# Performance work log

Hardware: AMD Instinct MI355X
Metric: run time of the kernel (lower is better)

## Reference

```python
import jax, jax.numpy as jnp
import numpy as np

N_NODES = 100000
IN_DIM = 128
HID = 128
N_EDGES = 1600000
N_PAIRS = 500000


def setup_inputs() -> dict:
    key = jax.random.key(0)
    ks = jax.random.split(key, 16)

    def lin(k, fan_out, fan_in):
        s = 1.0 / np.sqrt(fan_in)
        kw, kb = jax.random.split(k)
        W = jax.random.uniform(kw, (fan_out, fan_in), jnp.float32, -s, s)
        b = jax.random.uniform(kb, (fan_out,), jnp.float32, -s, s)
        return W, b

    x = jax.random.normal(ks[0], (N_NODES, IN_DIM), jnp.float32)
    edge_index = jax.random.randint(ks[1], (2, N_EDGES), 0, N_NODES, jnp.int64)
    edge_pairs = jax.random.randint(ks[2], (N_PAIRS, 2), 0, N_NODES, jnp.int64)

    # SAGEConv 1: lin_l (neighbor aggr, with bias), lin_r (root, no bias)
    W1l, b1l = lin(ks[3], HID, IN_DIM)
    W1r, _ = lin(ks[4], HID, IN_DIM)
    # SAGEConv 2
    W2l, b2l = lin(ks[5], HID, HID)
    W2r, _ = lin(ks[6], HID, HID)
    # MLP decoder
    Wm1, bm1 = lin(ks[7], HID, HID)
    Wm2, bm2 = lin(ks[8], HID // 2, HID)
    Wm3, bm3 = lin(ks[9], 1, HID // 2)

    return dict(x=x, edge_index=edge_index, edge_pairs=edge_pairs,
                W1l=W1l, b1l=b1l, W1r=W1r,
                W2l=W2l, b2l=b2l, W2r=W2r,
                Wm1=Wm1, bm1=bm1, Wm2=Wm2, bm2=bm2, Wm3=Wm3, bm3=bm3)


def _sage_conv(x, src, dst, Wl, bl, Wr):
    # mean aggregation of source-node features into destination nodes
    msg_sum = jax.ops.segment_sum(x[src], dst, num_segments=N_NODES)  # [N, D]
    cnt = jax.ops.segment_sum(jnp.ones((src.shape[0],), x.dtype), dst,
                              num_segments=N_NODES)
    aggr = msg_sum / jnp.maximum(cnt, 1.0)[:, None]
    return aggr @ Wl.T + bl + x @ Wr.T


def reference(x, edge_index, edge_pairs,
              W1l, b1l, W1r, W2l, b2l, W2r,
              Wm1, bm1, Wm2, bm2, Wm3, bm3):
    src, dst = edge_index[0], edge_index[1]
    # encode (eval mode: dropout = identity)
    h = jax.nn.relu(_sage_conv(x, src, dst, W1l, b1l, W1r))
    z = _sage_conv(h, src, dst, W2l, b2l, W2r)  # [N, HID]
    # decode
    hp = z[edge_pairs[:, 0]] * z[edge_pairs[:, 1]]  # [P, HID]
    hp = jax.nn.relu(hp @ Wm1.T + bm1)
    hp = jax.nn.relu(hp @ Wm2.T + bm2)
    return (hp @ Wm3.T + bm3).squeeze(-1)  # [P]
```

## Files before the change

### kernel.cpp

```cpp
#include <hip/hip_runtime.h>
#include <stdint.h>

typedef _Float16 half8 __attribute__((ext_vector_type(8)));
typedef float float4v __attribute__((ext_vector_type(4)));

constexpr int kN = 100000;
constexpr int kE = 1600000;
constexpr int kP = 500000;
constexpr int NBS = (kN + 255) / 256;
constexpr int CT3 = kN / 16;
constexpr int DT2 = kP / 32;

__global__ void prep_kernel(
    const int* __restrict__ dst, int* __restrict__ deg, int* __restrict__ slot,
    const float* __restrict__ x, _Float16* __restrict__ xh,
    const float* __restrict__ W1l, const float* __restrict__ W1r,
    const float* __restrict__ W2l, const float* __restrict__ W2r,
    const float* __restrict__ Wm1, const float* __restrict__ Wm2,
    _Float16* __restrict__ CW1h, _Float16* __restrict__ CW1e,
    _Float16* __restrict__ CW2h, _Float16* __restrict__ CW2e,
    _Float16* __restrict__ M1h,  _Float16* __restrict__ M2h)
{
    const int b = blockIdx.x;
    if (b < 6250) {
        const int e = b * 256 + threadIdx.x;
        if (e < kE) slot[e] = atomicAdd(&deg[dst[e]], 1);
    } else if (b < 12500) {
        const int i = ((b - 6250) * 256 + threadIdx.x) * 8;
        if (i >= kN * 128) return;
        const float4 a = *(const float4*)&x[i];
        const float4 bb = *(const float4*)&x[i + 4];
        half8 v;
        v[0] = (_Float16)a.x;  v[1] = (_Float16)a.y;  v[2] = (_Float16)a.z;  v[3] = (_Float16)a.w;
        v[4] = (_Float16)bb.x; v[5] = (_Float16)bb.y; v[6] = (_Float16)bb.z; v[7] = (_Float16)bb.w;
        *(half8*)&xh[i] = v;
    } else {
        const int i = (b - 12500) * 256 + threadIdx.x;
        if (i < 32768) {
            const int o = i >> 8, k = i & 255;
            const float w = (k < 128) ? W1l[o * 128 + k] : W1r[o * 128 + k - 128];
            const _Float16 h = (_Float16)w;
            CW1h[i] = h; CW1e[i] = (_Float16)(w - (float)h);
        } else if (i < 65536) {
            const int j = i - 32768;
            const int o = j >> 8, k = j & 255;
            const float w = (k < 128) ? W2l[o * 128 + k] : W2r[o * 128 + k - 128];
            const _Float16 h = (_Float16)w;
            CW2h[j] = h; CW2e[j] = (_Float16)(w - (float)h);
        } else if (i < 81920) {
            const int j = i - 65536;
            M1h[j] = (_Float16)Wm1[j];
        } else if (i < 90112) {
            const int j = i - 81920;
            M2h[j] = (_Float16)Wm2[j];
        }
    }
}

__global__ void scan_block_sums(const int* __restrict__ deg, int* __restrict__ bsum) {
    __shared__ int red[256];
    int t = threadIdx.x;
    int i = blockIdx.x * 256 + t;
    red[t] = (i < kN) ? deg[i] : 0;
    __syncthreads();
    for (int s = 128; s > 0; s >>= 1) {
        if (t < s) red[t] += red[t + s];
        __syncthreads();
    }
    if (t == 0) bsum[blockIdx.x] = red[0];
}

__global__ void scan_bsums(const int* __restrict__ bsum, int* __restrict__ boff) {
    __shared__ int sm[512];
    int t = threadIdx.x;
    int orig = (t < NBS) ? bsum[t] : 0;
    sm[t] = orig;
    __syncthreads();
    for (int d = 1; d < 512; d <<= 1) {
        int u = (t >= d) ? sm[t - d] : 0;
        __syncthreads();
        sm[t] += u;
        __syncthreads();
    }
    if (t < NBS) boff[t] = sm[t] - orig;
}

__global__ void scan_write(const int* __restrict__ deg, const int* __restrict__ boff,
                           int* __restrict__ row_start) {
    __shared__ int sm[256];
    int t = threadIdx.x;
    int i = blockIdx.x * 256 + t;
    int v = (i < kN) ? deg[i] : 0;
    sm[t] = v;
    __syncthreads();
    for (int d = 1; d < 256; d <<= 1) {
        int u = (t >= d) ? sm[t - d] : 0;
        __syncthreads();
        sm[t] += u;
        __syncthreads();
    }
    int excl = sm[t] - v + boff[blockIdx.x];
    if (i < kN) row_start[i] = excl;
    if (i == kN - 1) row_start[kN] = excl + v;
}

__global__ void fill2_kernel(const int* __restrict__ src, const int* __restrict__ dst,
                             const int* __restrict__ row_start,
                             const int* __restrict__ slot, int* __restrict__ srcs) {
    int e = blockIdx.x * blockDim.x + threadIdx.x;
    if (e < kE) srcs[row_start[dst[e]] + slot[e]] = src[e];
}

template <bool RELU>
__global__ __launch_bounds__(64, 4) void conv_mfma(
    const _Float16* __restrict__ xin,
    const int* __restrict__ row_start,
    const int* __restrict__ srcs,
    const _Float16* __restrict__ Wh,
    const _Float16* __restrict__ We,
    const float* __restrict__ bias,
    _Float16* __restrict__ out)
{
    __shared__ __align__(16) _Float16 stg[16 * 136];
    const int l = threadIdx.x & 63;
    const int p = l & 15;
    const int q = l >> 4;
    const int tile = blockIdx.x;
    const int c = p * 8;
    const int lbase = l & 48;

    int j0[4], j1[4];
#pragma unroll
    for (int s = 0; s < 4; s++) {
        const int n = tile * 16 + s * 4 + q;
        j0[s] = row_start[n];
        j1[s] = row_start[n + 1];
    }
    int idx16[4];
#pragma unroll
    for (int s = 0; s < 4; s++) {
        const int tA = j0[s] + p;
        const int v  = srcs[tA];
        idx16[s] = (tA < j1[s]) ? v : 0;
    }

#pragma unroll
    for (int s = 0; s < 4; s++) {
        const int cnt = j1[s] - j0[s];
        float facc[8];
#pragma unroll
        for (int u = 0; u < 8; u++) facc[u] = 0.f;

        for (int jc = j0[s]; jc < j1[s]; jc += 16) {
            int myidx;
            if (jc == j0[s]) {
                myidx = idx16[s];
            } else {
                const int tB = jc + p;
                const int v  = srcs[tB];
                myidx = (tB < j1[s]) ? v : 0;
            }
            half8 rows[16];
#pragma unroll
            for (int i = 0; i < 16; i++) {
                const int sidx = __shfl(myidx, lbase + i);
                rows[i] = *(const half8*)&xin[(size_t)sidx * 128 + c];
            }
            __builtin_amdgcn_sched_barrier(0);
            const int rem = j1[s] - jc;
#pragma unroll
            for (int i = 0; i < 16; i++) {
                if (i < rem) {
#pragma unroll
                    for (int u = 0; u < 8; u++) facc[u] += (float)rows[i][u];
                }
            }
        }
        const float inv = 1.0f / (float)(cnt > 1 ? cnt : 1);
        half8 hv;
#pragma unroll
        for (int u = 0; u < 8; u++) hv[u] = (_Float16)(facc[u] * inv);
        *(half8*)&stg[(s * 4 + q) * 136 + c] = hv;
    }

    half8 rt[4];
#pragma unroll
    for (int kt = 0; kt < 4; kt++)
        rt[kt] = *(const half8*)&xin[(size_t)(tile * 16 + p) * 128 + kt * 32 + q * 8];

    half8 am[4];
#pragma unroll
    for (int kt = 0; kt < 4; kt++)
        am[kt] = *(const half8*)&stg[p * 136 + kt * 32 + q * 8];

    float4v acc[8];
#pragma unroll
    for (int nt = 0; nt < 8; nt++) {
        const float b = bias[nt * 16 + p];
        acc[nt][0] = b; acc[nt][1] = b; acc[nt][2] = b; acc[nt][3] = b;
    }
#pragma unroll
    for (int kt = 0; kt < 8; kt++) {
        const half8 a = (kt < 4) ? am[kt] : rt[kt - 4];
#pragma unroll
        for (int nt = 0; nt < 8; nt++) {
            const int widx = (nt * 16 + p) * 256 + kt * 32 + q * 8;
            const half8 bh = *(const half8*)&Wh[widx];
            const half8 be = *(const half8*)&We[widx];
            acc[nt] = __builtin_amdgcn_mfma_f32_16x16x32_f16(a, bh, acc[nt], 0, 0, 0);
            acc[nt] = __builtin_amdgcn_mfma_f32_16x16x32_f16(a, be, acc[nt], 0, 0, 0);
        }
    }

#pragma unroll
    for (int nt = 0; nt < 8; nt++)
#pragma unroll
        for (int r = 0; r < 4; r++) {
            float v = acc[nt][r];
            if (RELU) v = fmaxf(v, 0.f);
            stg[(q * 4 + r) * 136 + nt * 16 + p] = (_Float16)v;
        }
    {
        const int row = l >> 2;
        const int c2  = (l & 3) * 8;
#pragma unroll
        for (int i = 0; i < 4; i++)
            *(half8*)&out[(size_t)(tile * 16 + row) * 128 + i * 32 + c2] =
                *(const half8*)&stg[row * 136 + i * 32 + c2];
    }
}

__global__ __launch_bounds__(64, 4) void decoder_mfma(
    const _Float16* __restrict__ z,
    const int* __restrict__ pairs,
    const _Float16* __restrict__ M1h, const float* __restrict__ bm1,
    const _Float16* __restrict__ M2h, const float* __restrict__ bm2,
    const float* __restrict__ Wm3, const float* __restrict__ bm3,
    float* __restrict__ outv)
{
    __shared__ __align__(16) _Float16 buf[32 * 136];
    const int l = threadIdx.x & 63;
    const int p = l & 15;
    const int q = l >> 4;
    const int tile = blockIdx.x;
    const int c = p * 8;

    int2 ab[8];
#pragma unroll
    for (int it = 0; it < 8; it++)
        ab[it] = *(const int2*)&pairs[(size_t)(tile * 32 + it * 4 + q) * 2];
    half8 za[8], zb[8];
#pragma unroll
    for (int it = 0; it < 8; it++) {
        za[it] = *(const half8*)&z[(size_t)ab[it].x * 128 + c];
        zb[it] = *(const half8*)&z[(size_t)ab[it].y * 128 + c];
    }
    __builtin_amdgcn_sched_barrier(0);
#pragma unroll
    for (int it = 0; it < 8; it++)
        *(half8*)&buf[(it * 4 + q) * 136 + c] = za[it] * zb[it];

    half8 a1[2][4];
#pragma unroll
    for (int m = 0; m < 2; m++)
#pragma unroll
        for (int kt = 0; kt < 4; kt++)
            a1[m][kt] = *(const half8*)&buf[(m * 16 + p) * 136 + kt * 32 + q * 8];

    float4v acc1[2][8];
#pragma unroll
    for (int nt = 0; nt < 8; nt++) {
        const float b = bm1[nt * 16 + p];
#pragma unroll
        for (int m = 0; m < 2; m++) {
            acc1[m][nt][0] = b; acc1[m][nt][1] = b; acc1[m][nt][2] = b; acc1[m][nt][3] = b;
        }
    }
#pragma unroll
    for (int kt = 0; kt < 4; kt++)
#pragma unroll
        for (int nt = 0; nt < 8; nt++) {
            const half8 bh = *(const half8*)&M1h[(nt * 16 + p) * 128 + kt * 32 + q * 8];
            acc1[0][nt] = __builtin_amdgcn_mfma_f32_16x16x32_f16(a1[0][kt], bh, acc1[0][nt], 0, 0, 0);
            acc1[1][nt] = __builtin_amdgcn_mfma_f32_16x16x32_f16(a1[1][kt], bh, acc1[1][nt], 0, 0, 0);
        }

#pragma unroll
    for (int m = 0; m < 2; m++)
#pragma unroll
        for (int nt = 0; nt < 8; nt++)
#pragma unroll
            for (int r = 0; r < 4; r++)
                buf[(m * 16 + q * 4 + r) * 136 + nt * 16 + p] =
                    (_Float16)fmaxf(acc1[m][nt][r], 0.f);

    half8 a2[2][4];
#pragma unroll
    for (int m = 0; m < 2; m++)
#pragma unroll
        for (int kt = 0; kt < 4; kt++)
            a2[m][kt] = *(const half8*)&buf[(m * 16 + p) * 136 + kt * 32 + q * 8];

    float4v acc2[2][4];
#pragma unroll
    for (int nt = 0; nt < 4; nt++) {
        const float b = bm2[nt * 16 + p];
#pragma unroll
        for (int m = 0; m < 2; m++) {
            acc2[m][nt][0] = b; acc2[m][nt][1] = b; acc2[m][nt][2] = b; acc2[m][nt][3] = b;
        }
    }
#pragma unroll
    for (int kt = 0; kt < 4; kt++)
#pragma unroll
        for (int nt = 0; nt < 4; nt++) {
            const half8 bh = *(const half8*)&M2h[(nt * 16 + p) * 128 + kt * 32 + q * 8];
            acc2[0][nt] = __builtin_amdgcn_mfma_f32_16x16x32_f16(a2[0][kt], bh, acc2[0][nt], 0, 0, 0);
            acc2[1][nt] = __builtin_amdgcn_mfma_f32_16x16x32_f16(a2[1][kt], bh, acc2[1][nt], 0, 0, 0);
        }

    float wm3v[4];
#pragma unroll
    for (int nt = 0; nt < 4; nt++) wm3v[nt] = Wm3[nt * 16 + p];
    const float b3 = bm3[0];
#pragma unroll
    for (int m = 0; m < 2; m++) {
        float part[4];
#pragma unroll
        for (int r = 0; r < 4; r++) part[r] = 0.f;
#pragma unroll
        for (int nt = 0; nt < 4; nt++)
#pragma unroll
            for (int r = 0; r < 4; r++)
                part[r] += fmaxf(acc2[m][nt][r], 0.f) * wm3v[nt];
#pragma unroll
        for (int s = 1; s <= 8; s <<= 1)
#pragma unroll
            for (int r = 0; r < 4; r++) part[r] += __shfl_xor(part[r], s);
        if (p == 0) {
            float4 o = make_float4(part[0] + b3, part[1] + b3, part[2] + b3, part[3] + b3);
            *(float4*)&outv[tile * 32 + m * 16 + q * 4] = o;
        }
    }
}

extern "C" void kernel_launch(void* const* d_in, const int* in_sizes, int n_in,
                              void* d_out, int out_size, void* d_ws, size_t ws_size,
                              hipStream_t stream) {
    const float* x   = (const float*)d_in[0];
    const int*   src = (const int*)d_in[1];
    const int*   dst = src + kE;
    const int*   ep  = (const int*)d_in[2];
    const float* W1l = (const float*)d_in[3];
    const float* b1l = (const float*)d_in[4];
    const float* W1r = (const float*)d_in[5];
    const float* W2l = (const float*)d_in[6];
    const float* b2l = (const float*)d_in[7];
    const float* W2r = (const float*)d_in[8];
    const float* Wm1 = (const float*)d_in[9];
    const float* bm1 = (const float*)d_in[10];
    const float* Wm2 = (const float*)d_in[11];
    const float* bm2 = (const float*)d_in[12];
    const float* Wm3 = (const float*)d_in[13];
    const float* bm3 = (const float*)d_in[14];
    float* outv = (float*)d_out;

    char* ws = (char*)d_ws;
    size_t off = 0;
    auto alloc = [&](size_t bytes) -> void* {
        void* p = ws + off;
        off += bytes;
        off = (off + 255) & ~(size_t)255;
        return p;
    };
    int*      deg       = (int*)alloc((size_t)kN * 4);
    int*      row_start = (int*)alloc((size_t)(kN + 1) * 4);
    int*      slot      = (int*)alloc((size_t)kE * 4);
    int*      bsum      = (int*)alloc(512 * 4);
    int*      boff      = (int*)alloc(512 * 4);
    int*      srcs      = (int*)alloc((size_t)(kE + 64) * 4);
    _Float16* xh        = (_Float16*)alloc((size_t)kN * 128 * 2);
    _Float16* hh        = (_Float16*)alloc((size_t)kN * 128 * 2);
    _Float16* zh        = (_Float16*)alloc((size_t)kN * 128 * 2);
    _Float16* CW1h      = (_Float16*)alloc(128 * 256 * 2);
    _Float16* CW1e      = (_Float16*)alloc(128 * 256 * 2);
    _Float16* CW2h      = (_Float16*)alloc(128 * 256 * 2);
    _Float16* CW2e      = (_Float16*)alloc(128 * 256 * 2);
    _Float16* M1h       = (_Float16*)alloc(128 * 128 * 2);
    _Float16* M2h       = (_Float16*)alloc(64 * 128 * 2);

    hipMemsetAsync(deg, 0, (size_t)kN * sizeof(int), stream);
    prep_kernel<<<12852, 256, 0, stream>>>(dst, deg, slot, x, xh,
                                           W1l, W1r, W2l, W2r, Wm1, Wm2,
                                           CW1h, CW1e, CW2h, CW2e, M1h, M2h);
    scan_block_sums<<<NBS, 256, 0, stream>>>(deg, bsum);
    scan_bsums<<<1, 512, 0, stream>>>(bsum, boff);
    scan_write<<<NBS, 256, 0, stream>>>(deg, boff, row_start);
    fill2_kernel<<<(kE + 255) / 256, 256, 0, stream>>>(src, dst, row_start, slot, srcs);

    conv_mfma<true><<<CT3, 64, 0, stream>>>(xh, row_start, srcs, CW1h, CW1e, b1l, hh);
    conv_mfma<false><<<CT3, 64, 0, stream>>>(hh, row_start, srcs, CW2h, CW2e, b2l, zh);

    decoder_mfma<<<DT2, 64, 0, stream>>>(
        zh, ep, M1h, bm1, M2h, bm2, Wm3, bm3, outv);
}
```

Baseline: 607.5 us.

## Bucket-sort decoder pairs by first node and remap tiles per XCD for locality

Pairs are counting-sorted into bins of 32 consecutive first-node ids using a histogram built in the prep kernel, a single-block scan and a scatter pass. The decoder reads the sorted pairs, scatters results back through the saved original indices, and remaps block ids so each XCD handles a contiguous range of sorted tiles. The aim is better L2 reuse of the z rows gathered for the first endpoint on each XCD. The cost is two extra kernels, extra atomics, about 8 MB of extra traffic, and scattered 4-byte output stores.

```diff
diff --git a/kernel.cpp b/kernel.cpp
--- a/kernel.cpp
+++ b/kernel.cpp
@@ -10,6 +10,9 @@
 constexpr int NBS = (kN + 255) / 256;
 constexpr int CT3 = kN / 16;
 constexpr int DT2 = kP / 32;
+constexpr int PBINS = 3125;
+constexpr int PBINS_PAD = 3328;
+constexpr int PHB = (kP + 255) / 256;
 
 __global__ void prep_kernel(
     const int* __restrict__ dst, int* __restrict__ deg, int* __restrict__ slot,
@@ -19,7 +22,8 @@
     const float* __restrict__ Wm1, const float* __restrict__ Wm2,
     _Float16* __restrict__ CW1h, _Float16* __restrict__ CW1e,
     _Float16* __restrict__ CW2h, _Float16* __restrict__ CW2e,
-    _Float16* __restrict__ M1h,  _Float16* __restrict__ M2h)
+    _Float16* __restrict__ M1h,  _Float16* __restrict__ M2h,
+    const int* __restrict__ ep, int* __restrict__ phist, int* __restrict__ pslot)
 {
     const int b = blockIdx.x;
     if (b < 6250) {
@@ -34,7 +38,7 @@
         v[0] = (_Float16)a.x;  v[1] = (_Float16)a.y;  v[2] = (_Float16)a.z;  v[3] = (_Float16)a.w;
         v[4] = (_Float16)bb.x; v[5] = (_Float16)bb.y; v[6] = (_Float16)bb.z; v[7] = (_Float16)bb.w;
         *(half8*)&xh[i] = v;
-    } else {
+    } else if (b < 12852) {
         const int i = (b - 12500) * 256 + threadIdx.x;
         if (i < 32768) {
             const int o = i >> 8, k = i & 255;
@@ -54,6 +58,54 @@
             const int j = i - 81920;
             M2h[j] = (_Float16)Wm2[j];
         }
+    } else {
+        const int i = (b - 12852) * 256 + threadIdx.x;
+        if (i < kP) {
+            const int a = ep[(size_t)i * 2];
+            pslot[i] = atomicAdd(&phist[a >> 5], 1);
+        }
+    }
+}
+
+__global__ void psort_scan(const int* __restrict__ phist, int* __restrict__ pbase) {
+    __shared__ int sm[1024];
+    const int t = threadIdx.x;
+    int v[4];
+    int s = 0;
+#pragma unroll
+    for (int r = 0; r < 4; r++) {
+        const int bi = t * 4 + r;
+        v[r] = (bi < PBINS) ? phist[bi] : 0;
+        s += v[r];
+    }
+    sm[t] = s;
+    __syncthreads();
+    for (int d = 1; d < 1024; d <<= 1) {
+        int u = (t >= d) ? sm[t - d] : 0;
+        __syncthreads();
+        sm[t] += u;
+        __syncthreads();
+    }
+    int excl = sm[t] - s;
+#pragma unroll
+    for (int r = 0; r < 4; r++) {
+        const int bi = t * 4 + r;
+        if (bi < PBINS) pbase[bi] = excl;
+        excl += v[r];
+    }
+}
+
+__global__ void psort_scatter(const int* __restrict__ ep,
+                              const int* __restrict__ pbase,
+                              const int* __restrict__ pslot,
+                              int2* __restrict__ spair, int* __restrict__ sidx) {
+    const int i = blockIdx.x * 256 + threadIdx.x;
+    if (i < kP) {
+        const int a = ep[(size_t)i * 2];
+        const int bb = ep[(size_t)i * 2 + 1];
+        const int pos = pbase[a >> 5] + pslot[i];
+        spair[pos] = make_int2(a, bb);
+        sidx[pos] = i;
     }
 }
 
@@ -232,7 +284,8 @@
 
 __global__ __launch_bounds__(64, 4) void decoder_mfma(
     const _Float16* __restrict__ z,
-    const int* __restrict__ pairs,
+    const int2* __restrict__ spair,
+    const int* __restrict__ sidx,
     const _Float16* __restrict__ M1h, const float* __restrict__ bm1,
     const _Float16* __restrict__ M2h, const float* __restrict__ bm2,
     const float* __restrict__ Wm3, const float* __restrict__ bm3,
@@ -242,13 +295,16 @@
     const int l = threadIdx.x & 63;
     const int p = l & 15;
     const int q = l >> 4;
-    const int tile = blockIdx.x;
+    constexpr int qc = DT2 / 8, rc = DT2 % 8;
+    const int orig = blockIdx.x;
+    const int xcd = orig & 7, i8 = orig >> 3;
+    const int tile = (xcd < rc ? xcd * (qc + 1) : rc * (qc + 1) + (xcd - rc) * qc) + i8;
     const int c = p * 8;
 
     int2 ab[8];
 #pragma unroll
     for (int it = 0; it < 8; it++)
-        ab[it] = *(const int2*)&pairs[(size_t)(tile * 32 + it * 4 + q) * 2];
+        ab[it] = spair[tile * 32 + it * 4 + q];
     half8 za[8], zb[8];
 #pragma unroll
     for (int it = 0; it < 8; it++) {
@@ -338,8 +394,12 @@
 #pragma unroll
             for (int r = 0; r < 4; r++) part[r] += __shfl_xor(part[r], s);
         if (p == 0) {
-            float4 o = make_float4(part[0] + b3, part[1] + b3, part[2] + b3, part[3] + b3);
-            *(float4*)&outv[tile * 32 + m * 16 + q * 4] = o;
+            const int base = tile * 32 + m * 16 + q * 4;
+            const int4 oi = *(const int4*)&sidx[base];
+            outv[oi.x] = part[0] + b3;
+            outv[oi.y] = part[1] + b3;
+            outv[oi.z] = part[2] + b3;
+            outv[oi.w] = part[3] + b3;
         }
     }
 }
@@ -374,10 +434,15 @@
         return p;
     };
     int*      deg       = (int*)alloc((size_t)kN * 4);
+    int*      phist     = (int*)alloc((size_t)PBINS_PAD * 4);
     int*      row_start = (int*)alloc((size_t)(kN + 1) * 4);
     int*      slot      = (int*)alloc((size_t)kE * 4);
     int*      bsum      = (int*)alloc(512 * 4);
     int*      boff      = (int*)alloc(512 * 4);
+    int*      pbase     = (int*)alloc((size_t)PBINS_PAD * 4);
+    int*      pslot     = (int*)alloc((size_t)kP * 4);
+    int2*     spair     = (int2*)alloc((size_t)kP * 8);
+    int*      sidx      = (int*)alloc((size_t)kP * 4);
     int*      srcs      = (int*)alloc((size_t)(kE + 64) * 4);
     _Float16* xh        = (_Float16*)alloc((size_t)kN * 128 * 2);
     _Float16* hh        = (_Float16*)alloc((size_t)kN * 128 * 2);
@@ -389,10 +454,16 @@
     _Float16* M1h       = (_Float16*)alloc(128 * 128 * 2);
     _Float16* M2h       = (_Float16*)alloc(64 * 128 * 2);
 
-    hipMemsetAsync(deg, 0, (size_t)kN * sizeof(int), stream);
-    prep_kernel<<<12852, 256, 0, stream>>>(dst, deg, slot, x, xh,
-                                           W1l, W1r, W2l, W2r, Wm1, Wm2,
-                                           CW1h, CW1e, CW2h, CW2e, M1h, M2h);
+    const size_t z0 = (size_t)((char*)(phist + PBINS_PAD) - (char*)deg);
+    hipMemsetAsync(deg, 0, z0, stream);
+
+    prep_kernel<<<12852 + PHB, 256, 0, stream>>>(dst, deg, slot, x, xh,
+                                                 W1l, W1r, W2l, W2r, Wm1, Wm2,
+                                                 CW1h, CW1e, CW2h, CW2e, M1h, M2h,
+                                                 ep, phist, pslot);
+    psort_scan<<<1, 1024, 0, stream>>>(phist, pbase);
+    psort_scatter<<<PHB, 256, 0, stream>>>(ep, pbase, pslot, spair, sidx);
+
     scan_block_sums<<<NBS, 256, 0, stream>>>(deg, bsum);
     scan_bsums<<<1, 512, 0, stream>>>(bsum, boff);
     scan_write<<<NBS, 256, 0, stream>>>(deg, boff, row_start);
@@ -402,5 +473,5 @@
     conv_mfma<false><<<CT3, 64, 0, stream>>>(hh, row_start, srcs, CW2h, CW2e, b2l, zh);
 
     decoder_mfma<<<DT2, 64, 0, stream>>>(
-        zh, ep, M1h, bm1, M2h, bm2, Wm3, bm3, outv);
-}
+        zh, spair, sidx, M1h, bm1, M2h, bm2, Wm3, bm3, outv);
+}
```

After: 655.8 us. +8.0%, slower.
